# Performance work log

Hardware: AMD Instinct MI355X
Metric: run time of the kernel (lower is better)

The kernel has to match this reference:

```python
import jax, jax.numpy as jnp
import numpy as np

EMBED_DIM = 512
NUM_HEADS = 8
HEAD_DIM = EMBED_DIM // NUM_HEADS
PAIR_DIM = 64
B, L = 2, 1024


def setup_inputs() -> dict:
    key = jax.random.key(0)
    ks = jax.random.split(key, 6)
    seq_repr = jax.random.normal(ks[0], (B, L, EMBED_DIM), dtype=jnp.float32)
    pair_repr = jax.random.normal(ks[1], (B, L, L, PAIR_DIM), dtype=jnp.float32)
    # Parameters (stored as [in, out] for x @ W)
    sc = 0.02
    W_qkv = jax.random.normal(ks[2], (EMBED_DIM, 3 * EMBED_DIM), dtype=jnp.float32) * sc
    W_bias = jax.random.normal(ks[3], (PAIR_DIM, NUM_HEADS), dtype=jnp.float32) * sc
    W_out = jax.random.normal(ks[4], (EMBED_DIM, EMBED_DIM), dtype=jnp.float32) * sc
    b_out = jax.random.normal(ks[5], (EMBED_DIM,), dtype=jnp.float32) * sc
    return {"seq_repr": seq_repr, "pair_repr": pair_repr,
            "W_qkv": W_qkv, "W_bias": W_bias, "W_out": W_out, "b_out": b_out}


def reference(seq_repr, pair_repr, W_qkv, W_bias, W_out, b_out):
    b, l, _ = seq_repr.shape
    # pair bias: [B, L, L, pair_dim] -> [B, H, L, L]
    pair_bias = jnp.einsum('bijp,ph->bhij', pair_repr, W_bias)
    qkv = seq_repr @ W_qkv                      # [B, L, 3*E]
    q, k, v = jnp.split(qkv, 3, axis=-1)
    def heads(x):
        return x.reshape(b, l, NUM_HEADS, HEAD_DIM).transpose(0, 2, 1, 3)  # [B,H,L,D]
    q, k, v = heads(q), heads(k), heads(v)
    scale = 1.0 / jnp.sqrt(jnp.asarray(HEAD_DIM, dtype=q.dtype))
    scores = jnp.einsum('bhid,bhjd->bhij', q, k) * scale + pair_bias
    attn = jax.nn.softmax(scores, axis=-1)
    ctx = jnp.einsum('bhij,bhjd->bhid', attn, v)             # [B,H,L,D]
    ctx = ctx.transpose(0, 2, 1, 3).reshape(b, l, EMBED_DIM)
    return ctx @ W_out + b_out
```

## Files before the change

### kernel.cpp

```cpp
#include <hip/hip_runtime.h>
#include <hip/hip_bf16.h>


typedef __attribute__((ext_vector_type(8))) short bf16x8;
typedef __attribute__((ext_vector_type(4))) float f32x4;

__device__ __forceinline__ unsigned pk2(float a, float b) {
    __hip_bfloat16 ha = __float2bfloat16(a);
    __hip_bfloat16 hb = __float2bfloat16(b);
    return (unsigned)__bfloat16_as_ushort(ha) | ((unsigned)__bfloat16_as_ushort(hb) << 16);
}

__device__ __forceinline__ void gl16_nt(const void* g, void* l) {
    __builtin_amdgcn_global_load_lds((const __attribute__((address_space(1))) void*)g,
                                     (__attribute__((address_space(3))) void*)l, 16, 0, 2);
}

__global__ __launch_bounds__(256, 2) void gemm_qkv_kernel(
    const float* __restrict__ A, const float* __restrict__ W,
    unsigned short* __restrict__ qbus, unsigned short* __restrict__ kbus,
    unsigned short* __restrict__ vtbus)
{
    __shared__ float smem[64 * 68];
    float* As = smem;
    float* Bs = smem + 32 * 68;

    const int t  = threadIdx.x;
    const int m0 = blockIdx.y * 64;
    const int n0 = blockIdx.x * 64;
    const int tx = t & 15, ty = t >> 4;

    const int am = t >> 2, ak = (t & 3) * 8;
    const int bk = t >> 3, bn = (t & 7) * 8;

    float acc[4][4] = {};

    for (int k0 = 0; k0 < 512; k0 += 32) {
        float4 a0 = *(const float4*)&A[(size_t)(m0 + am) * 512 + k0 + ak];
        float4 a1 = *(const float4*)&A[(size_t)(m0 + am) * 512 + k0 + ak + 4];
        float4 b0 = *(const float4*)&W[(size_t)(k0 + bk) * 1536 + n0 + bn];
        float4 b1 = *(const float4*)&W[(size_t)(k0 + bk) * 1536 + n0 + bn + 4];
        __syncthreads();
        As[(ak + 0) * 68 + am] = a0.x;
        As[(ak + 1) * 68 + am] = a0.y;
        As[(ak + 2) * 68 + am] = a0.z;
        As[(ak + 3) * 68 + am] = a0.w;
        As[(ak + 4) * 68 + am] = a1.x;
        As[(ak + 5) * 68 + am] = a1.y;
        As[(ak + 6) * 68 + am] = a1.z;
        As[(ak + 7) * 68 + am] = a1.w;
        *(float4*)&Bs[bk * 68 + bn]     = b0;
        *(float4*)&Bs[bk * 68 + bn + 4] = b1;
        __syncthreads();
#pragma unroll
        for (int kk = 0; kk < 32; kk++) {
            float4 a4 = *(float4*)&As[kk * 68 + ty * 4];
            float4 b4 = *(float4*)&Bs[kk * 68 + tx * 4];
            float av[4] = {a4.x, a4.y, a4.z, a4.w};
            float bv[4] = {b4.x, b4.y, b4.z, b4.w};
#pragma unroll
            for (int r = 0; r < 4; r++)
#pragma unroll
                for (int c = 0; c < 4; c++) acc[r][c] += av[r] * bv[c];
        }
    }

    const int sect = n0 >> 9;
    const int h    = (n0 >> 6) & 7;
    const int b    = m0 >> 10;
    const int i0   = m0 & 1023;

    if (sect == 2) {
        __syncthreads();
        float* T = smem;
#pragma unroll
        for (int r = 0; r < 4; r++)
#pragma unroll
            for (int c = 0; c < 4; c++)
                T[(tx * 4 + c) * 68 + (ty * 4 + r)] = acc[r][c];
        __syncthreads();
        const int dp = t >> 2, iq = (t & 3) * 16;
        unsigned short* dst = vtbus + (((size_t)(b * 8 + h)) * 64 + dp) * 1024 + i0 + iq;
#pragma unroll
        for (int u = 0; u < 4; u++) {
            float4 f = *(float4*)&T[dp * 68 + iq + u * 4];
            uint2 pkd; pkd.x = pk2(f.x, f.y); pkd.y = pk2(f.z, f.w);
            *(uint2*)&dst[u * 4] = pkd;
        }
    } else {
        unsigned short* dst = (sect == 0) ? qbus : kbus;
        const float sc = (sect == 0) ? 0.125f : 1.0f;
#pragma unroll
        for (int r = 0; r < 4; r++) {
            const int i = i0 + ty * 4 + r;
#pragma unroll
            for (int c = 0; c < 4; c += 2) {
                unsigned u = pk2(acc[r][c] * sc, acc[r][c + 1] * sc);
                *(unsigned*)&dst[(((size_t)(b * 8 + h)) * 1024 + i) * 64 + tx * 4 + c] = u;
            }
        }
    }
}

__device__ __forceinline__ bf16x8 slab_frag(const char* rowb, int ks, int q4, int sw) {
    const int s0 = ks * 8 + q4 * 2;
    const float4 fa = *(const float4*)(rowb + (((s0    ) ^ sw) << 4));
    const float4 fb = *(const float4*)(rowb + (((s0 + 1) ^ sw) << 4));
    uint4 u;
    u.x = pk2(fa.x, fa.y); u.y = pk2(fa.z, fa.w);
    u.z = pk2(fb.x, fb.y); u.w = pk2(fb.z, fb.w);
    return *(bf16x8*)&u;
}

__global__ __launch_bounds__(512, 4) void attn_kernel(
    const float* __restrict__ pair, const float* __restrict__ Wb,
    const unsigned short* __restrict__ qbus, const unsigned short* __restrict__ kbus,
    const unsigned short* __restrict__ vtbus, float* __restrict__ cp,
    float* __restrict__ mlm, float* __restrict__ mll)
{
    __shared__ __align__(16) char plds[2][32768];
    __shared__ __align__(16) float bias_lds[128 * 17];
    __shared__ __align__(16) unsigned short pbuf[8 * 16 * 24];

    const int t    = threadIdx.x;
    const int lane = t & 63;
    const int w    = t >> 6;
    const int q4   = lane >> 4;
    const int l15  = lane & 15;

    const int bx   = blockIdx.x;
    const int vbid = ((bx & 7) << 6) | (bx >> 3);
    const int b    = vbid >> 8;
    const int rem  = vbid & 255;
    const int jh   = rem >> 7;
    const int i0   = (rem & 127) * 8;

    uint4 wbf[2];
#pragma unroll
    for (int ks = 0; ks < 2; ks++) {
        float f[8];
#pragma unroll
        for (int e = 0; e < 8; e++)
            f[e] = (l15 < 8) ? Wb[(ks * 32 + q4 * 8 + e) * 8 + l15] : 0.f;
        wbf[ks].x = pk2(f[0], f[1]); wbf[ks].y = pk2(f[2], f[3]);
        wbf[ks].z = pk2(f[4], f[5]); wbf[ks].w = pk2(f[6], f[7]);
    }

    uint4 qf[2] = {};
    if (l15 < 8) {
        const unsigned short* qrow = qbus + (size_t)((b * 8 + w) * 1024 + i0 + l15) * 64;
#pragma unroll
        for (int ks = 0; ks < 2; ks++)
            qf[ks] = *(const uint4*)(qrow + ks * 32 + q4 * 8);
    }

    const int rb = w * 4 + q4;
    const char* pairB = (const char*)pair + (size_t)(b * 1024 + i0) * 262144
                      + (size_t)jh * 131072
                      + (rb >> 4) * 262144 + (rb & 15) * 256 + ((l15 ^ (rb & 15)) << 4);
    char* ldsW = (char*)plds + w * 1024;

#define STAGE(bufsel, jtn) do {                                         \
        const char* gg = pairB + (size_t)(jtn) * 4096;                  \
        char* ld = ldsW + (bufsel) * 32768;                             \
        _Pragma("unroll")                                               \
        for (int r = 0; r < 4; r++)                                     \
            gl16_nt(gg + (size_t)r * 524288, ld + r * 8192);            \
    } while (0)

    STAGE(0, 0);

    f32x4 acc[4];
#pragma unroll
    for (int dn = 0; dn < 4; dn++) acc[dn] = (f32x4){0.f, 0.f, 0.f, 0.f};
    float mrun[4], lrun[4];
#pragma unroll
    for (int rr = 0; rr < 4; rr++) { mrun[rr] = -3.0e38f; lrun[rr] = 0.f; }

    const unsigned short* kbase = kbus + (size_t)((b * 8 + w) * 1024 + jh * 512) * 64;
    const unsigned short* vbase = vtbus + (size_t)((b * 8 + w) * 64) * 1024 + jh * 512;

    for (int jt = 0; jt < 32; jt++) {
        asm volatile("s_waitcnt vmcnt(0) lgkmcnt(0)" ::: "memory");
        __builtin_amdgcn_sched_barrier(0);
        __builtin_amdgcn_s_barrier();
        __builtin_amdgcn_sched_barrier(0);

        const char* cur = (const char*)plds + (jt & 1) * 32768;

        uint4 kf[2], vf[4];
        {
            const unsigned short* kt = kbase + (size_t)(jt * 16 + l15) * 64;
#pragma unroll
            for (int ks = 0; ks < 2; ks++)
                kf[ks] = *(const uint4*)(kt + ks * 32 + q4 * 8);
#pragma unroll
            for (int dn = 0; dn < 4; dn++)
                vf[dn] = *(const uint4*)(vbase + (size_t)(dn * 16 + l15) * 1024
                                         + jt * 16 + (q4 & 1) * 8);
        }

        if (jt < 31) STAGE((jt + 1) & 1, jt + 1);

        {
            const char* rb0 = cur + (32 * w + l15) * 256;
            const char* rb1 = cur + (32 * w + 16 + l15) * 256;
            f32x4 b0 = {0.f, 0.f, 0.f, 0.f}, b1 = {0.f, 0.f, 0.f, 0.f};
#pragma unroll
            for (int ks = 0; ks < 2; ks++) {
                bf16x8 a0 = slab_frag(rb0, ks, q4, l15);
                b0 = __builtin_amdgcn_mfma_f32_16x16x32_bf16(a0, *(bf16x8*)&wbf[ks], b0, 0, 0, 0);
                bf16x8 a1 = slab_frag(rb1, ks, q4, l15);
                b1 = __builtin_amdgcn_mfma_f32_16x16x32_bf16(a1, *(bf16x8*)&wbf[ks], b1, 0, 0, 0);
            }
            if (l15 < 8) {
#pragma unroll
                for (int rr = 0; rr < 4; rr++) {
                    bias_lds[(32 * w + q4 * 4 + rr) * 17 + l15]      = b0[rr];
                    bias_lds[(32 * w + 16 + q4 * 4 + rr) * 17 + l15] = b1[rr];
                }
            }
        }

        asm volatile("s_waitcnt lgkmcnt(0)" ::: "memory");
        __builtin_amdgcn_sched_barrier(0);
        __builtin_amdgcn_s_barrier();
        __builtin_amdgcn_sched_barrier(0);

        f32x4 s;
#pragma unroll
        for (int rr = 0; rr < 4; rr++)
            s[rr] = (q4 < 2) ? bias_lds[((q4 * 4 + rr) * 16 + l15) * 17 + w] : 0.f;
        s = __builtin_amdgcn_mfma_f32_16x16x32_bf16(*(bf16x8*)&qf[0], *(bf16x8*)&kf[0], s, 0, 0, 0);
        s = __builtin_amdgcn_mfma_f32_16x16x32_bf16(*(bf16x8*)&qf[1], *(bf16x8*)&kf[1], s, 0, 0, 0);

#pragma unroll
        for (int rr = 0; rr < 4; rr++) {
            float x = s[rr];
            x = fmaxf(x, __shfl_xor(x, 1));
            x = fmaxf(x, __shfl_xor(x, 2));
            x = fmaxf(x, __shfl_xor(x, 4));
            x = fmaxf(x, __shfl_xor(x, 8));
            const float mnew = fmaxf(mrun[rr], x);
            const float corr = __expf(mrun[rr] - mnew);
            mrun[rr] = mnew;
            const float p0 = __expf(s[rr] - mnew);
            float ts = p0;
            ts += __shfl_xor(ts, 1);
            ts += __shfl_xor(ts, 2);
            ts += __shfl_xor(ts, 4);
            ts += __shfl_xor(ts, 8);
            lrun[rr] = lrun[rr] * corr + ts;
#pragma unroll
            for (int dn = 0; dn < 4; dn++) acc[dn][rr] *= corr;
            pbuf[(w * 16 + q4 * 4 + rr) * 24 + l15] =
                __bfloat16_as_ushort(__float2bfloat16(p0));
        }

        asm volatile("s_waitcnt lgkmcnt(0)" ::: "memory");
        __builtin_amdgcn_sched_barrier(0);

        bf16x8 pfrag = (bf16x8){0, 0, 0, 0, 0, 0, 0, 0};
        if (q4 < 2) pfrag = *(bf16x8*)&pbuf[(w * 16 + l15) * 24 + q4 * 8];
#pragma unroll
        for (int dn = 0; dn < 4; dn++)
            acc[dn] = __builtin_amdgcn_mfma_f32_16x16x32_bf16(pfrag, *(bf16x8*)&vf[dn], acc[dn], 0, 0, 0);
    }

    if (q4 < 2) {
#pragma unroll
        for (int rr = 0; rr < 4; rr++) {
            const int i = q4 * 4 + rr;
            float* crow = cp + (size_t)jh * (2048 * 512)
                        + ((size_t)(b * 1024) + i0 + i) * 512 + w * 64;
#pragma unroll
            for (int dn = 0; dn < 4; dn++)
                crow[dn * 16 + l15] = acc[dn][rr];
            if (l15 == 0) {
                const int mi = ((jh * 2 + b) * 8 + w) * 1024 + i0 + i;
                mlm[mi] = mrun[rr];
                mll[mi] = lrun[rr];
            }
        }
    }
#undef STAGE
}

__global__ __launch_bounds__(256) void merge_kernel(
    const float* __restrict__ cp, const float* __restrict__ mlm,
    const float* __restrict__ mll, float* __restrict__ ctx)
{
    const int row = blockIdx.x;
    const int b   = row >> 10, i = row & 1023;
    const int t   = threadIdx.x;
    const int h   = t >> 5;

    const int mi0 = ((0 * 2 + b) * 8 + h) * 1024 + i;
    const int mi1 = ((1 * 2 + b) * 8 + h) * 1024 + i;
    const float m0 = mlm[mi0], m1 = mlm[mi1];
    const float l0 = mll[mi0], l1 = mll[mi1];
    const float M  = fmaxf(m0, m1);
    const float w0 = __expf(m0 - M), w1 = __expf(m1 - M);
    const float inv = 1.0f / (l0 * w0 + l1 * w1);

    const float2 c0 = *(const float2*)&cp[(size_t)row * 512 + t * 2];
    const float2 c1 = *(const float2*)&cp[(size_t)(2048 * 512) + (size_t)row * 512 + t * 2];
    float2 o;
    o.x = (c0.x * w0 + c1.x * w1) * inv;
    o.y = (c0.y * w0 + c1.y * w1) * inv;
    *(float2*)&ctx[(size_t)row * 512 + t * 2] = o;
}

__global__ __launch_bounds__(256, 2) void gemm_out_kernel(
    const float* __restrict__ A, const float* __restrict__ W,
    const float* __restrict__ bias, float* __restrict__ out)
{
    __shared__ float smem[64 * 68];
    float* As = smem;
    float* Bs = smem + 32 * 68;

    const int t  = threadIdx.x;
    const int m0 = blockIdx.y * 64;
    const int n0 = blockIdx.x * 64;
    const int tx = t & 15, ty = t >> 4;

    const int am = t >> 2, ak = (t & 3) * 8;
    const int bk = t >> 3, bn = (t & 7) * 8;

    float acc[4][4] = {};

    for (int k0 = 0; k0 < 512; k0 += 32) {
        float4 a0 = *(const float4*)&A[(size_t)(m0 + am) * 512 + k0 + ak];
        float4 a1 = *(const float4*)&A[(size_t)(m0 + am) * 512 + k0 + ak + 4];
        float4 b0 = *(const float4*)&W[(size_t)(k0 + bk) * 512 + n0 + bn];
        float4 b1 = *(const float4*)&W[(size_t)(k0 + bk) * 512 + n0 + bn + 4];
        __syncthreads();
        As[(ak + 0) * 68 + am] = a0.x;
        As[(ak + 1) * 68 + am] = a0.y;
        As[(ak + 2) * 68 + am] = a0.z;
        As[(ak + 3) * 68 + am] = a0.w;
        As[(ak + 4) * 68 + am] = a1.x;
        As[(ak + 5) * 68 + am] = a1.y;
        As[(ak + 6) * 68 + am] = a1.z;
        As[(ak + 7) * 68 + am] = a1.w;
        *(float4*)&Bs[bk * 68 + bn]     = b0;
        *(float4*)&Bs[bk * 68 + bn + 4] = b1;
        __syncthreads();
#pragma unroll
        for (int kk = 0; kk < 32; kk++) {
            float4 a4 = *(float4*)&As[kk * 68 + ty * 4];
            float4 b4 = *(float4*)&Bs[kk * 68 + tx * 4];
            float av[4] = {a4.x, a4.y, a4.z, a4.w};
            float bv[4] = {b4.x, b4.y, b4.z, b4.w};
#pragma unroll
            for (int r = 0; r < 4; r++)
#pragma unroll
                for (int c = 0; c < 4; c++) acc[r][c] += av[r] * bv[c];
        }
    }

    float4 bo = *(const float4*)&bias[n0 + tx * 4];
    float bv[4] = {bo.x, bo.y, bo.z, bo.w};
#pragma unroll
    for (int r = 0; r < 4; r++) {
        const int m = m0 + ty * 4 + r;
#pragma unroll
        for (int c = 0; c < 4; c++)
            out[(size_t)m * 512 + n0 + tx * 4 + c] = acc[r][c] + bv[c];
    }
}

extern "C" void kernel_launch(void* const* d_in, const int* in_sizes, int n_in,
                              void* d_out, int out_size, void* d_ws, size_t ws_size,
                              hipStream_t stream)
{
    const float* seq  = (const float*)d_in[0];
    const float* pair = (const float*)d_in[1];
    const float* Wqkv = (const float*)d_in[2];
    const float* Wb   = (const float*)d_in[3];
    const float* Wout = (const float*)d_in[4];
    const float* bout = (const float*)d_in[5];
    float* out = (float*)d_out;

    unsigned short* qbus  = (unsigned short*)d_ws;
    unsigned short* kbus  = qbus + (1 << 20);
    unsigned short* vtbus = kbus + (1 << 20);
    float*          ctx   = (float*)(vtbus + (1 << 20));
    float*          cp    = ctx + (1 << 20);
    float*          mlm   = cp + (2 << 20);
    float*          mll   = mlm + (1 << 15);

    gemm_qkv_kernel<<<dim3(24, 32), 256, 0, stream>>>(seq, Wqkv, qbus, kbus, vtbus);
    attn_kernel<<<512, 512, 0, stream>>>(pair, Wb, qbus, kbus, vtbus, cp, mlm, mll);
    merge_kernel<<<2048, 256, 0, stream>>>(cp, mlm, mll, ctx);
    gemm_out_kernel<<<dim3(8, 32), 256, 0, stream>>>(ctx, Wout, bout, out);
}
```

Before: 236.2 us.

## Split pair-bias projection into separate kernel and widen attention tiles

Moves the pair_repr x W_bias projection out of the attention kernel into a dedicated bias_kernel that streams the 512MB-class pair tensor and writes a bf16 [B,H,L,L] bias buffer. The attention kernel then reads precomputed bias, drops the LDS double-buffered pair staging and block barriers, and processes 16 query rows and 32 keys per step, so all MFMA lanes are used. This trades an extra write and read of the bias buffer (bf16, 32MB) for simpler, barrier-free attention with better MFMA utilization. It also adds one kernel launch and removes the overlap between the pair stream and the attention math.

```diff
diff --git a/kernel.cpp b/kernel.cpp
--- a/kernel.cpp
+++ b/kernel.cpp
@@ -4,16 +4,13 @@
 
 typedef __attribute__((ext_vector_type(8))) short bf16x8;
 typedef __attribute__((ext_vector_type(4))) float f32x4;
+
+#define BFLO(u) __uint_as_float(((unsigned)(u)) << 16)
 
 __device__ __forceinline__ unsigned pk2(float a, float b) {
     __hip_bfloat16 ha = __float2bfloat16(a);
     __hip_bfloat16 hb = __float2bfloat16(b);
     return (unsigned)__bfloat16_as_ushort(ha) | ((unsigned)__bfloat16_as_ushort(hb) << 16);
-}
-
-__device__ __forceinline__ void gl16_nt(const void* g, void* l) {
-    __builtin_amdgcn_global_load_lds((const __attribute__((address_space(1))) void*)g,
-                                     (__attribute__((address_space(3))) void*)l, 16, 0, 2);
 }
 
 __global__ __launch_bounds__(256, 2) void gemm_qkv_kernel(
@@ -102,25 +99,63 @@
     }
 }
 
-__device__ __forceinline__ bf16x8 slab_frag(const char* rowb, int ks, int q4, int sw) {
-    const int s0 = ks * 8 + q4 * 2;
-    const float4 fa = *(const float4*)(rowb + (((s0    ) ^ sw) << 4));
-    const float4 fb = *(const float4*)(rowb + (((s0 + 1) ^ sw) << 4));
-    uint4 u;
-    u.x = pk2(fa.x, fa.y); u.y = pk2(fa.z, fa.w);
-    u.z = pk2(fb.x, fb.y); u.w = pk2(fb.z, fb.w);
-    return *(bf16x8*)&u;
-}
-
-__global__ __launch_bounds__(512, 4) void attn_kernel(
+__global__ __launch_bounds__(256) void bias_kernel(
     const float* __restrict__ pair, const float* __restrict__ Wb,
-    const unsigned short* __restrict__ qbus, const unsigned short* __restrict__ kbus,
-    const unsigned short* __restrict__ vtbus, float* __restrict__ cp,
-    float* __restrict__ mlm, float* __restrict__ mll)
-{
-    __shared__ __align__(16) char plds[2][32768];
-    __shared__ __align__(16) float bias_lds[128 * 17];
-    __shared__ __align__(16) unsigned short pbuf[8 * 16 * 24];
+    unsigned short* __restrict__ biasb)
+{
+    const int t    = threadIdx.x;
+    const int lane = t & 63;
+    const int wv   = t >> 6;
+    const int q4   = lane >> 4;
+    const int l15  = lane & 15;
+
+    uint4 wbf[2];
+#pragma unroll
+    for (int ks = 0; ks < 2; ks++) {
+        float f[8];
+#pragma unroll
+        for (int e = 0; e < 8; e++)
+            f[e] = (l15 < 8) ? Wb[(ks * 32 + q4 * 8 + e) * 8 + l15] : 0.f;
+        wbf[ks].x = pk2(f[0], f[1]); wbf[ks].y = pk2(f[2], f[3]);
+        wbf[ks].z = pk2(f[4], f[5]); wbf[ks].w = pk2(f[6], f[7]);
+    }
+
+    const int u = blockIdx.x * 4 + wv;
+#pragma unroll 1
+    for (int g = 0; g < 16; g++) {
+        const size_t Gi = (size_t)u * 16 + g;
+        const size_t r0 = Gi * 16;
+        const float* rp = pair + (r0 + l15) * 64;
+
+        f32x4 c = {0.f, 0.f, 0.f, 0.f};
+#pragma unroll
+        for (int ks = 0; ks < 2; ks++) {
+            float4 fa = *(const float4*)(rp + ks * 32 + q4 * 8);
+            float4 fb = *(const float4*)(rp + ks * 32 + q4 * 8 + 4);
+            uint4 af;
+            af.x = pk2(fa.x, fa.y); af.y = pk2(fa.z, fa.w);
+            af.z = pk2(fb.x, fb.y); af.w = pk2(fb.z, fb.w);
+            c = __builtin_amdgcn_mfma_f32_16x16x32_bf16(*(bf16x8*)&af, *(bf16x8*)&wbf[ks], c, 0, 0, 0);
+        }
+
+        if (l15 < 8) {
+            const int b   = (int)(r0 >> 20);
+            const int i   = (int)((r0 >> 10) & 1023);
+            const int j0g = (int)(r0 & 1023);
+            unsigned short* dp = biasb + ((((size_t)(b * 8 + l15)) * 1024 + i) << 10)
+                               + j0g + q4 * 4;
+            *(unsigned*)dp       = pk2(c[0], c[1]);
+            *(unsigned*)(dp + 2) = pk2(c[2], c[3]);
+        }
+    }
+}
+
+__global__ __launch_bounds__(512, 2) void attn_kernel(
+    const unsigned short* __restrict__ biasb, const unsigned short* __restrict__ qbus,
+    const unsigned short* __restrict__ kbus, const unsigned short* __restrict__ vtbus,
+    float* __restrict__ cp, float* __restrict__ mlm, float* __restrict__ mll)
+{
+    __shared__ __align__(16) unsigned short pbuf[8 * 16 * 40];
 
     const int t    = threadIdx.x;
     const int lane = t & 63;
@@ -129,47 +164,20 @@
     const int l15  = lane & 15;
 
     const int bx   = blockIdx.x;
-    const int vbid = ((bx & 7) << 6) | (bx >> 3);
-    const int b    = vbid >> 8;
-    const int rem  = vbid & 255;
-    const int jh   = rem >> 7;
-    const int i0   = (rem & 127) * 8;
-
-    uint4 wbf[2];
-#pragma unroll
-    for (int ks = 0; ks < 2; ks++) {
-        float f[8];
-#pragma unroll
-        for (int e = 0; e < 8; e++)
-            f[e] = (l15 < 8) ? Wb[(ks * 32 + q4 * 8 + e) * 8 + l15] : 0.f;
-        wbf[ks].x = pk2(f[0], f[1]); wbf[ks].y = pk2(f[2], f[3]);
-        wbf[ks].z = pk2(f[4], f[5]); wbf[ks].w = pk2(f[6], f[7]);
-    }
-
-    uint4 qf[2] = {};
-    if (l15 < 8) {
+    const int vbid = ((bx & 7) << 5) | (bx >> 3);
+    const int b    = vbid >> 7;
+    const int rem  = vbid & 127;
+    const int jh   = rem >> 6;
+    const int i0   = (rem & 63) * 16;
+
+    uint4 qf[2];
+    {
         const unsigned short* qrow = qbus + (size_t)((b * 8 + w) * 1024 + i0 + l15) * 64;
 #pragma unroll
         for (int ks = 0; ks < 2; ks++)
             qf[ks] = *(const uint4*)(qrow + ks * 32 + q4 * 8);
     }
 
-    const int rb = w * 4 + q4;
-    const char* pairB = (const char*)pair + (size_t)(b * 1024 + i0) * 262144
-                      + (size_t)jh * 131072
-                      + (rb >> 4) * 262144 + (rb & 15) * 256 + ((l15 ^ (rb & 15)) << 4);
-    char* ldsW = (char*)plds + w * 1024;
-
-#define STAGE(bufsel, jtn) do {                                         \
-        const char* gg = pairB + (size_t)(jtn) * 4096;                  \
-        char* ld = ldsW + (bufsel) * 32768;                             \
-        _Pragma("unroll")                                               \
-        for (int r = 0; r < 4; r++)                                     \
-            gl16_nt(gg + (size_t)r * 524288, ld + r * 8192);            \
-    } while (0)
-
-    STAGE(0, 0);
-
     f32x4 acc[4];
 #pragma unroll
     for (int dn = 0; dn < 4; dn++) acc[dn] = (f32x4){0.f, 0.f, 0.f, 0.f};
@@ -179,64 +187,40 @@
 
     const unsigned short* kbase = kbus + (size_t)((b * 8 + w) * 1024 + jh * 512) * 64;
     const unsigned short* vbase = vtbus + (size_t)((b * 8 + w) * 64) * 1024 + jh * 512;
-
-    for (int jt = 0; jt < 32; jt++) {
-        asm volatile("s_waitcnt vmcnt(0) lgkmcnt(0)" ::: "memory");
-        __builtin_amdgcn_sched_barrier(0);
-        __builtin_amdgcn_s_barrier();
-        __builtin_amdgcn_sched_barrier(0);
-
-        const char* cur = (const char*)plds + (jt & 1) * 32768;
-
-        uint4 kf[2], vf[4];
+    const unsigned short* bbase = biasb + ((size_t)((b * 8 + w) * 1024 + i0)) * 1024 + jh * 512;
+
+    for (int jt = 0; jt < 16; jt++) {
+        const int j0 = jt * 32;
+
+        f32x4 s0, s1;
+#pragma unroll
+        for (int rr = 0; rr < 4; rr++) {
+            const unsigned short* bp = bbase + (size_t)(q4 * 4 + rr) * 1024 + j0;
+            s0[rr] = BFLO(bp[l15]);
+            s1[rr] = BFLO(bp[16 + l15]);
+        }
+
+        uint4 kf[2][2], vf[4];
         {
-            const unsigned short* kt = kbase + (size_t)(jt * 16 + l15) * 64;
-#pragma unroll
-            for (int ks = 0; ks < 2; ks++)
-                kf[ks] = *(const uint4*)(kt + ks * 32 + q4 * 8);
+            const unsigned short* kt = kbase + (size_t)(j0 + l15) * 64;
+#pragma unroll
+            for (int jn = 0; jn < 2; jn++)
+#pragma unroll
+                for (int ks = 0; ks < 2; ks++)
+                    kf[jn][ks] = *(const uint4*)(kt + jn * 16 * 64 + ks * 32 + q4 * 8);
 #pragma unroll
             for (int dn = 0; dn < 4; dn++)
-                vf[dn] = *(const uint4*)(vbase + (size_t)(dn * 16 + l15) * 1024
-                                         + jt * 16 + (q4 & 1) * 8);
-        }
-
-        if (jt < 31) STAGE((jt + 1) & 1, jt + 1);
-
-        {
-            const char* rb0 = cur + (32 * w + l15) * 256;
-            const char* rb1 = cur + (32 * w + 16 + l15) * 256;
-            f32x4 b0 = {0.f, 0.f, 0.f, 0.f}, b1 = {0.f, 0.f, 0.f, 0.f};
-#pragma unroll
-            for (int ks = 0; ks < 2; ks++) {
-                bf16x8 a0 = slab_frag(rb0, ks, q4, l15);
-                b0 = __builtin_amdgcn_mfma_f32_16x16x32_bf16(a0, *(bf16x8*)&wbf[ks], b0, 0, 0, 0);
-                bf16x8 a1 = slab_frag(rb1, ks, q4, l15);
-                b1 = __builtin_amdgcn_mfma_f32_16x16x32_bf16(a1, *(bf16x8*)&wbf[ks], b1, 0, 0, 0);
-            }
-            if (l15 < 8) {
-#pragma unroll
-                for (int rr = 0; rr < 4; rr++) {
-                    bias_lds[(32 * w + q4 * 4 + rr) * 17 + l15]      = b0[rr];
-                    bias_lds[(32 * w + 16 + q4 * 4 + rr) * 17 + l15] = b1[rr];
-                }
-            }
-        }
-
-        asm volatile("s_waitcnt lgkmcnt(0)" ::: "memory");
-        __builtin_amdgcn_sched_barrier(0);
-        __builtin_amdgcn_s_barrier();
-        __builtin_amdgcn_sched_barrier(0);
-
-        f32x4 s;
-#pragma unroll
-        for (int rr = 0; rr < 4; rr++)
-            s[rr] = (q4 < 2) ? bias_lds[((q4 * 4 + rr) * 16 + l15) * 17 + w] : 0.f;
-        s = __builtin_amdgcn_mfma_f32_16x16x32_bf16(*(bf16x8*)&qf[0], *(bf16x8*)&kf[0], s, 0, 0, 0);
-        s = __builtin_amdgcn_mfma_f32_16x16x32_bf16(*(bf16x8*)&qf[1], *(bf16x8*)&kf[1], s, 0, 0, 0);
+                vf[dn] = *(const uint4*)(vbase + (size_t)(dn * 16 + l15) * 1024 + j0 + q4 * 8);
+        }
+
+        s0 = __builtin_amdgcn_mfma_f32_16x16x32_bf16(*(bf16x8*)&qf[0], *(bf16x8*)&kf[0][0], s0, 0, 0, 0);
+        s0 = __builtin_amdgcn_mfma_f32_16x16x32_bf16(*(bf16x8*)&qf[1], *(bf16x8*)&kf[0][1], s0, 0, 0, 0);
+        s1 = __builtin_amdgcn_mfma_f32_16x16x32_bf16(*(bf16x8*)&qf[0], *(bf16x8*)&kf[1][0], s1, 0, 0, 0);
+        s1 = __builtin_amdgcn_mfma_f32_16x16x32_bf16(*(bf16x8*)&qf[1], *(bf16x8*)&kf[1][1], s1, 0, 0, 0);
 
 #pragma unroll
         for (int rr = 0; rr < 4; rr++) {
-            float x = s[rr];
+            float x = fmaxf(s0[rr], s1[rr]);
             x = fmaxf(x, __shfl_xor(x, 1));
             x = fmaxf(x, __shfl_xor(x, 2));
             x = fmaxf(x, __shfl_xor(x, 4));
@@ -244,8 +228,9 @@
             const float mnew = fmaxf(mrun[rr], x);
             const float corr = __expf(mrun[rr] - mnew);
             mrun[rr] = mnew;
-            const float p0 = __expf(s[rr] - mnew);
-            float ts = p0;
+            const float p0 = __expf(s0[rr] - mnew);
+            const float p1 = __expf(s1[rr] - mnew);
+            float ts = p0 + p1;
             ts += __shfl_xor(ts, 1);
             ts += __shfl_xor(ts, 2);
             ts += __shfl_xor(ts, 4);
@@ -253,37 +238,37 @@
             lrun[rr] = lrun[rr] * corr + ts;
 #pragma unroll
             for (int dn = 0; dn < 4; dn++) acc[dn][rr] *= corr;
-            pbuf[(w * 16 + q4 * 4 + rr) * 24 + l15] =
-                __bfloat16_as_ushort(__float2bfloat16(p0));
+            unsigned short* pb = &pbuf[(w * 16 + q4 * 4 + rr) * 40];
+            pb[l15]      = __bfloat16_as_ushort(__float2bfloat16(p0));
+            pb[16 + l15] = __bfloat16_as_ushort(__float2bfloat16(p1));
         }
 
         asm volatile("s_waitcnt lgkmcnt(0)" ::: "memory");
         __builtin_amdgcn_sched_barrier(0);
 
-        bf16x8 pfrag = (bf16x8){0, 0, 0, 0, 0, 0, 0, 0};
-        if (q4 < 2) pfrag = *(bf16x8*)&pbuf[(w * 16 + l15) * 24 + q4 * 8];
+        bf16x8 pfrag = *(bf16x8*)&pbuf[(w * 16 + l15) * 40 + q4 * 8];
+        asm volatile("s_waitcnt lgkmcnt(0)" ::: "memory");
+        __builtin_amdgcn_sched_barrier(0);
+
 #pragma unroll
         for (int dn = 0; dn < 4; dn++)
             acc[dn] = __builtin_amdgcn_mfma_f32_16x16x32_bf16(pfrag, *(bf16x8*)&vf[dn], acc[dn], 0, 0, 0);
     }
 
-    if (q4 < 2) {
-#pragma unroll
-        for (int rr = 0; rr < 4; rr++) {
-            const int i = q4 * 4 + rr;
-            float* crow = cp + (size_t)jh * (2048 * 512)
-                        + ((size_t)(b * 1024) + i0 + i) * 512 + w * 64;
-#pragma unroll
-            for (int dn = 0; dn < 4; dn++)
-                crow[dn * 16 + l15] = acc[dn][rr];
-            if (l15 == 0) {
-                const int mi = ((jh * 2 + b) * 8 + w) * 1024 + i0 + i;
-                mlm[mi] = mrun[rr];
-                mll[mi] = lrun[rr];
-            }
-        }
-    }
-#undef STAGE
+#pragma unroll
+    for (int rr = 0; rr < 4; rr++) {
+        const int i = q4 * 4 + rr;
+        float* crow = cp + (size_t)jh * (2048 * 512)
+                    + ((size_t)(b * 1024) + i0 + i) * 512 + w * 64;
+#pragma unroll
+        for (int dn = 0; dn < 4; dn++)
+            crow[dn * 16 + l15] = acc[dn][rr];
+        if (l15 == 0) {
+            const int mi = ((jh * 2 + b) * 8 + w) * 1024 + i0 + i;
+            mlm[mi] = mrun[rr];
+            mll[mi] = lrun[rr];
+        }
+    }
 }
 
 __global__ __launch_bounds__(256) void merge_kernel(
@@ -389,9 +374,11 @@
     float*          cp    = ctx + (1 << 20);
     float*          mlm   = cp + (2 << 20);
     float*          mll   = mlm + (1 << 15);
+    unsigned short* biasb = (unsigned short*)(mll + (1 << 15));
 
     gemm_qkv_kernel<<<dim3(24, 32), 256, 0, stream>>>(seq, Wqkv, qbus, kbus, vtbus);
-    attn_kernel<<<512, 512, 0, stream>>>(pair, Wb, qbus, kbus, vtbus, cp, mlm, mll);
+    bias_kernel<<<2048, 256, 0, stream>>>(pair, Wb, biasb);
+    attn_kernel<<<256, 512, 0, stream>>>(biasb, qbus, kbus, vtbus, cp, mlm, mll);
     merge_kernel<<<2048, 256, 0, stream>>>(cp, mlm, mll, ctx);
     gemm_out_kernel<<<dim3(8, 32), 256, 0, stream>>>(ctx, Wout, bout, out);
 }
```

New measurement: 248.7 us. +5.3%, slower.

## Restructure pair-bias staging per wave, relax sync, fuse merge into output GEMM

Applied to the files above, without the earlier changes.

Each wave now loads and projects its own 16 pair rows per tile, so the pair-bias MFMA work is halved per wave. The top-of-loop full vmcnt(0)+barrier is replaced by partial vmcnt waits and an end-of-loop barrier, letting K/V loads overlap. Bias values are stored as bf16 in LDS. The split-softmax merge kernel is folded into the output GEMM's A-tile load, which removes one launch and the ctx round trip. The cost is more global reads of cp inside the GEMM and slightly lower bias precision.

```diff
diff --git a/kernel.cpp b/kernel.cpp
--- a/kernel.cpp
+++ b/kernel.cpp
@@ -4,6 +4,8 @@
 
 typedef __attribute__((ext_vector_type(8))) short bf16x8;
 typedef __attribute__((ext_vector_type(4))) float f32x4;
+
+#define BFLO(u) __uint_as_float(((unsigned)(u)) << 16)
 
 __device__ __forceinline__ unsigned pk2(float a, float b) {
     __hip_bfloat16 ha = __float2bfloat16(a);
@@ -119,7 +121,7 @@
     float* __restrict__ mlm, float* __restrict__ mll)
 {
     __shared__ __align__(16) char plds[2][32768];
-    __shared__ __align__(16) float bias_lds[128 * 17];
+    __shared__ __align__(16) unsigned short bias_lds[128 * 17];
     __shared__ __align__(16) unsigned short pbuf[8 * 16 * 24];
 
     const int t    = threadIdx.x;
@@ -154,18 +156,25 @@
             qf[ks] = *(const uint4*)(qrow + ks * 32 + q4 * 8);
     }
 
-    const int rb = w * 4 + q4;
-    const char* pairB = (const char*)pair + (size_t)(b * 1024 + i0) * 262144
-                      + (size_t)jh * 131072
-                      + (rb >> 4) * 262144 + (rb & 15) * 256 + ((l15 ^ (rb & 15)) << 4);
-    char* ldsW = (char*)plds + w * 1024;
+    asm volatile("s_waitcnt vmcnt(0)" ::: "memory");
+    __builtin_amdgcn_sched_barrier(0);
+
+    const char* prow = (const char*)pair
+                     + ((size_t)(b * 1024 + i0 + w) * 1024 + jh * 512) * 256;
+    int soff[4];
+#pragma unroll
+    for (int r = 0; r < 4; r++) {
+        const int jl = r * 4 + q4;
+        soff[r] = jl * 256 + ((l15 ^ jl) << 4);
+    }
+    char* ldsW = (char*)plds + w * 4096;
 
 #define STAGE(bufsel, jtn) do {                                         \
-        const char* gg = pairB + (size_t)(jtn) * 4096;                  \
+        const char* gg = prow + (size_t)(jtn) * 4096;                   \
         char* ld = ldsW + (bufsel) * 32768;                             \
         _Pragma("unroll")                                               \
         for (int r = 0; r < 4; r++)                                     \
-            gl16_nt(gg + (size_t)r * 524288, ld + r * 8192);            \
+            gl16_nt(gg + soff[r], ld + r * 1024);                       \
     } while (0)
 
     STAGE(0, 0);
@@ -180,45 +189,41 @@
     const unsigned short* kbase = kbus + (size_t)((b * 8 + w) * 1024 + jh * 512) * 64;
     const unsigned short* vbase = vtbus + (size_t)((b * 8 + w) * 64) * 1024 + jh * 512;
 
+#pragma unroll 1
     for (int jt = 0; jt < 32; jt++) {
-        asm volatile("s_waitcnt vmcnt(0) lgkmcnt(0)" ::: "memory");
-        __builtin_amdgcn_sched_barrier(0);
-        __builtin_amdgcn_s_barrier();
-        __builtin_amdgcn_sched_barrier(0);
-
         const char* cur = (const char*)plds + (jt & 1) * 32768;
 
         uint4 kf[2], vf[4];
         {
             const unsigned short* kt = kbase + (size_t)(jt * 16 + l15) * 64;
-#pragma unroll
-            for (int ks = 0; ks < 2; ks++)
-                kf[ks] = *(const uint4*)(kt + ks * 32 + q4 * 8);
+            kf[0] = *(const uint4*)(kt + q4 * 8);
+            kf[1] = *(const uint4*)(kt + 32 + q4 * 8);
 #pragma unroll
             for (int dn = 0; dn < 4; dn++)
                 vf[dn] = *(const uint4*)(vbase + (size_t)(dn * 16 + l15) * 1024
                                          + jt * 16 + (q4 & 1) * 8);
         }
 
-        if (jt < 31) STAGE((jt + 1) & 1, jt + 1);
+        if (jt < 31) {
+            STAGE((jt + 1) & 1, jt + 1);
+            asm volatile("s_waitcnt vmcnt(10)" ::: "memory");
+        } else {
+            asm volatile("s_waitcnt vmcnt(6)" ::: "memory");
+        }
+        __builtin_amdgcn_sched_barrier(0);
 
         {
-            const char* rb0 = cur + (32 * w + l15) * 256;
-            const char* rb1 = cur + (32 * w + 16 + l15) * 256;
-            f32x4 b0 = {0.f, 0.f, 0.f, 0.f}, b1 = {0.f, 0.f, 0.f, 0.f};
-#pragma unroll
-            for (int ks = 0; ks < 2; ks++) {
-                bf16x8 a0 = slab_frag(rb0, ks, q4, l15);
-                b0 = __builtin_amdgcn_mfma_f32_16x16x32_bf16(a0, *(bf16x8*)&wbf[ks], b0, 0, 0, 0);
-                bf16x8 a1 = slab_frag(rb1, ks, q4, l15);
-                b1 = __builtin_amdgcn_mfma_f32_16x16x32_bf16(a1, *(bf16x8*)&wbf[ks], b1, 0, 0, 0);
-            }
+            const char* rowb = cur + w * 4096 + l15 * 256;
+            f32x4 bb = {0.f, 0.f, 0.f, 0.f};
+#pragma unroll
+            for (int ks = 0; ks < 2; ks++)
+                bb = __builtin_amdgcn_mfma_f32_16x16x32_bf16(
+                        slab_frag(rowb, ks, q4, l15), *(bf16x8*)&wbf[ks], bb, 0, 0, 0);
             if (l15 < 8) {
 #pragma unroll
-                for (int rr = 0; rr < 4; rr++) {
-                    bias_lds[(32 * w + q4 * 4 + rr) * 17 + l15]      = b0[rr];
-                    bias_lds[(32 * w + 16 + q4 * 4 + rr) * 17 + l15] = b1[rr];
-                }
+                for (int rr = 0; rr < 4; rr++)
+                    bias_lds[(w * 16 + q4 * 4 + rr) * 17 + l15] =
+                        __bfloat16_as_ushort(__float2bfloat16(bb[rr]));
             }
         }
 
@@ -229,8 +234,10 @@
 
         f32x4 s;
 #pragma unroll
-        for (int rr = 0; rr < 4; rr++)
-            s[rr] = (q4 < 2) ? bias_lds[((q4 * 4 + rr) * 16 + l15) * 17 + w] : 0.f;
+        for (int rr = 0; rr < 4; rr++) {
+            const int ii = q4 * 4 + rr;
+            s[rr] = (q4 < 2) ? BFLO(bias_lds[(ii * 16 + l15) * 17 + w]) : 0.f;
+        }
         s = __builtin_amdgcn_mfma_f32_16x16x32_bf16(*(bf16x8*)&qf[0], *(bf16x8*)&kf[0], s, 0, 0, 0);
         s = __builtin_amdgcn_mfma_f32_16x16x32_bf16(*(bf16x8*)&qf[1], *(bf16x8*)&kf[1], s, 0, 0, 0);
 
@@ -265,6 +272,8 @@
 #pragma unroll
         for (int dn = 0; dn < 4; dn++)
             acc[dn] = __builtin_amdgcn_mfma_f32_16x16x32_bf16(pfrag, *(bf16x8*)&vf[dn], acc[dn], 0, 0, 0);
+
+        __builtin_amdgcn_s_barrier();
     }
 
     if (q4 < 2) {
@@ -286,33 +295,9 @@
 #undef STAGE
 }
 
-__global__ __launch_bounds__(256) void merge_kernel(
+__global__ __launch_bounds__(256, 2) void gemm_out_fused(
     const float* __restrict__ cp, const float* __restrict__ mlm,
-    const float* __restrict__ mll, float* __restrict__ ctx)
-{
-    const int row = blockIdx.x;
-    const int b   = row >> 10, i = row & 1023;
-    const int t   = threadIdx.x;
-    const int h   = t >> 5;
-
-    const int mi0 = ((0 * 2 + b) * 8 + h) * 1024 + i;
-    const int mi1 = ((1 * 2 + b) * 8 + h) * 1024 + i;
-    const float m0 = mlm[mi0], m1 = mlm[mi1];
-    const float l0 = mll[mi0], l1 = mll[mi1];
-    const float M  = fmaxf(m0, m1);
-    const float w0 = __expf(m0 - M), w1 = __expf(m1 - M);
-    const float inv = 1.0f / (l0 * w0 + l1 * w1);
-
-    const float2 c0 = *(const float2*)&cp[(size_t)row * 512 + t * 2];
-    const float2 c1 = *(const float2*)&cp[(size_t)(2048 * 512) + (size_t)row * 512 + t * 2];
-    float2 o;
-    o.x = (c0.x * w0 + c1.x * w1) * inv;
-    o.y = (c0.y * w0 + c1.y * w1) * inv;
-    *(float2*)&ctx[(size_t)row * 512 + t * 2] = o;
-}
-
-__global__ __launch_bounds__(256, 2) void gemm_out_kernel(
-    const float* __restrict__ A, const float* __restrict__ W,
+    const float* __restrict__ mll, const float* __restrict__ W,
     const float* __restrict__ bias, float* __restrict__ out)
 {
     __shared__ float smem[64 * 68];
@@ -327,22 +312,45 @@
     const int am = t >> 2, ak = (t & 3) * 8;
     const int bk = t >> 3, bn = (t & 7) * 8;
 
+    const int row = m0 + am;
+    const int bb  = row >> 10, ii = row & 1023;
+    const float* cp0 = cp + (size_t)row * 512;
+    const float* cp1 = cp + (size_t)(2048 * 512) + (size_t)row * 512;
+
     float acc[4][4] = {};
+    float w0 = 0.f, w1 = 0.f;
 
     for (int k0 = 0; k0 < 512; k0 += 32) {
-        float4 a0 = *(const float4*)&A[(size_t)(m0 + am) * 512 + k0 + ak];
-        float4 a1 = *(const float4*)&A[(size_t)(m0 + am) * 512 + k0 + ak + 4];
+        if ((k0 & 63) == 0) {
+            const int h   = k0 >> 6;
+            const int mi0 = ((bb) * 8 + h) * 1024 + ii;
+            const int mi1 = ((2 + bb) * 8 + h) * 1024 + ii;
+            const float m0_ = mlm[mi0], m1_ = mlm[mi1];
+            const float l0_ = mll[mi0], l1_ = mll[mi1];
+            const float M   = fmaxf(m0_, m1_);
+            float e0 = __expf(m0_ - M), e1 = __expf(m1_ - M);
+            const float inv = 1.0f / (l0_ * e0 + l1_ * e1);
+            w0 = e0 * inv; w1 = e1 * inv;
+        }
+        float4 c0a = *(const float4*)&cp0[k0 + ak];
+        float4 c0b = *(const float4*)&cp0[k0 + ak + 4];
+        float4 c1a = *(const float4*)&cp1[k0 + ak];
+        float4 c1b = *(const float4*)&cp1[k0 + ak + 4];
         float4 b0 = *(const float4*)&W[(size_t)(k0 + bk) * 512 + n0 + bn];
         float4 b1 = *(const float4*)&W[(size_t)(k0 + bk) * 512 + n0 + bn + 4];
-        __syncthreads();
-        As[(ak + 0) * 68 + am] = a0.x;
-        As[(ak + 1) * 68 + am] = a0.y;
-        As[(ak + 2) * 68 + am] = a0.z;
-        As[(ak + 3) * 68 + am] = a0.w;
-        As[(ak + 4) * 68 + am] = a1.x;
-        As[(ak + 5) * 68 + am] = a1.y;
-        As[(ak + 6) * 68 + am] = a1.z;
-        As[(ak + 7) * 68 + am] = a1.w;
+        float a0x = c0a.x * w0 + c1a.x * w1, a0y = c0a.y * w0 + c1a.y * w1;
+        float a0z = c0a.z * w0 + c1a.z * w1, a0w = c0a.w * w0 + c1a.w * w1;
+        float a1x = c0b.x * w0 + c1b.x * w1, a1y = c0b.y * w0 + c1b.y * w1;
+        float a1z = c0b.z * w0 + c1b.z * w1, a1w = c0b.w * w0 + c1b.w * w1;
+        __syncthreads();
+        As[(ak + 0) * 68 + am] = a0x;
+        As[(ak + 1) * 68 + am] = a0y;
+        As[(ak + 2) * 68 + am] = a0z;
+        As[(ak + 3) * 68 + am] = a0w;
+        As[(ak + 4) * 68 + am] = a1x;
+        As[(ak + 5) * 68 + am] = a1y;
+        As[(ak + 6) * 68 + am] = a1z;
+        As[(ak + 7) * 68 + am] = a1w;
         *(float4*)&Bs[bk * 68 + bn]     = b0;
         *(float4*)&Bs[bk * 68 + bn + 4] = b1;
         __syncthreads();
@@ -385,13 +393,11 @@
     unsigned short* qbus  = (unsigned short*)d_ws;
     unsigned short* kbus  = qbus + (1 << 20);
     unsigned short* vtbus = kbus + (1 << 20);
-    float*          ctx   = (float*)(vtbus + (1 << 20));
-    float*          cp    = ctx + (1 << 20);
+    float*          cp    = (float*)(vtbus + (1 << 20));
     float*          mlm   = cp + (2 << 20);
     float*          mll   = mlm + (1 << 15);
 
     gemm_qkv_kernel<<<dim3(24, 32), 256, 0, stream>>>(seq, Wqkv, qbus, kbus, vtbus);
     attn_kernel<<<512, 512, 0, stream>>>(pair, Wb, qbus, kbus, vtbus, cp, mlm, mll);
-    merge_kernel<<<2048, 256, 0, stream>>>(cp, mlm, mll, ctx);
-    gemm_out_kernel<<<dim3(8, 32), 256, 0, stream>>>(ctx, Wout, bout, out);
-}
+    gemm_out_fused<<<dim3(8, 32), 256, 0, stream>>>(cp, mlm, mll, Wout, bout, out);
+}
```

Measured after the change: 239.3 us. About the same (+1.3%).
